# Kernel optimization log

Hardware: AMD Instinct MI355X
Metric: run time of the kernel (lower is better)

The kernel has to match this reference:

```python
import jax, jax.numpy as jnp
import numpy as np
from jax import lax

B, N, H = 256, 512, 256


def setup_inputs() -> dict:
    key = jax.random.key(0)
    ks = jax.random.split(key, 8)
    s = 1.0 / np.sqrt(H)  # torch default init scale ~ U(-1/sqrt(H), 1/sqrt(H))
    return {
        "encoder_outputs": jax.random.normal(ks[0], (B, N, H), dtype=jnp.float32),
        "W_ih": jax.random.uniform(ks[1], (4 * H, H), jnp.float32, -s, s),
        "W_hh": jax.random.uniform(ks[2], (4 * H, H), jnp.float32, -s, s),
        "b_ih": jax.random.uniform(ks[3], (4 * H,), jnp.float32, -s, s),
        "b_hh": jax.random.uniform(ks[4], (4 * H,), jnp.float32, -s, s),
        "W_ref": jax.random.uniform(ks[5], (H, H), jnp.float32, -s, s),
        "W_q": jax.random.uniform(ks[6], (H, H), jnp.float32, -s, s),
        "v": jax.random.uniform(ks[7], (H,), jnp.float32, -s, s),
    }


def reference(encoder_outputs, W_ih, W_hh, b_ih, b_hh, W_ref, W_q, v):
    # Inference path (target_permutation=None): LSTM input at each step is the
    # previous hidden state; mask stays all-ones so masked_fill is a no-op.
    b, n, h = encoder_outputs.shape
    enc_proj = jnp.einsum('bnh,kh->bnk', encoder_outputs, W_ref)  # W_ref(encoder_outputs)

    def step(carry, _):
        hid, cell = carry
        # torch LSTMCell: gates = x W_ih^T + b_ih + h W_hh^T + b_hh, order (i,f,g,o)
        gates = hid @ W_ih.T + b_ih + hid @ W_hh.T + b_hh  # x == hid here
        i, f, g, o = jnp.split(gates, 4, axis=-1)
        cell = jax.nn.sigmoid(f) * cell + jax.nn.sigmoid(i) * jnp.tanh(g)
        hid = jax.nn.sigmoid(o) * jnp.tanh(cell)
        q = hid @ W_q.T                                    # [B,H]
        logits = jnp.tanh(enc_proj + q[:, None, :]) @ v    # [B,N]
        return (hid, cell), logits

    init = (jnp.zeros((b, h), encoder_outputs.dtype),
            jnp.zeros((b, h), encoder_outputs.dtype))
    _, logits_tn = lax.scan(step, init, None, length=n)    # [N,B,N]
    return jnp.transpose(logits_tn, (1, 0, 2))             # [B,N,N]
```

## Files before the change

### kernel.cpp

```cpp
#include <hip/hip_runtime.h>
#include <math.h>


#define CL2 2.8853900817779268f
#define LOG2E 1.4426950408889634f

#define YN0 0.98078528f
#define YN1 0.83146961f
#define YN2 0.55557023f
#define YN3 0.19509032f

#if __has_builtin(__builtin_amdgcn_exp2f)
__device__ __forceinline__ float fast_exp2(float x) { return __builtin_amdgcn_exp2f(x); }
#else
__device__ __forceinline__ float fast_exp2(float x) { return exp2f(x); }
#endif

#if __has_builtin(__builtin_amdgcn_rcpf)
__device__ __forceinline__ float fast_rcp(float x) { return __builtin_amdgcn_rcpf(x); }
#else
__device__ __forceinline__ float fast_rcp(float x) { return 1.0f / x; }
#endif

#if __has_builtin(__builtin_amdgcn_sdot4)
__device__ __forceinline__ int sdot4(int a, int b, int c) {
  return __builtin_amdgcn_sdot4(a, b, c, false);
}
#else
__device__ __forceinline__ int sdot4(int a, int b, int c) {
  c += (int)(signed char)(a)       * (int)(signed char)(b);
  c += (int)(signed char)(a >> 8)  * (int)(signed char)(b >> 8);
  c += (int)(signed char)(a >> 16) * (int)(signed char)(b >> 16);
  c += (int)(signed char)(a >> 24) * (int)(signed char)(b >> 24);
  return c;
}
#endif

typedef _Float16 f16x8 __attribute__((ext_vector_type(8)));
typedef float f32x4 __attribute__((ext_vector_type(4)));

__device__ __forceinline__ f16x8 as_f16x8(float4 x) {
  union { float4 f; f16x8 h; } u; u.f = x; return u.h;
}


__global__ void prep_kernel(const float* __restrict__ Wih, const float* __restrict__ Whh,
                            const float* __restrict__ bih, const float* __restrict__ bhh,
                            const float* __restrict__ Wref,
                            int* __restrict__ wpack, float* __restrict__ bsum,
                            unsigned short* __restrict__ Wrefsw) {
  const int bid = blockIdx.x, tid = threadIdx.x;
  if (bid < 256) {
    const int idx   = bid * 256 + tid;
    const int gidx  = idx & 3;
    const int chunk = (idx >> 2) & 15;
    const int qd    = (idx >> 6) & 255;
    const int sl    = idx >> 14;
    const int gate  = 4 * qd + gidx;
    const int k0    = 64 * sl + 4 * chunk;
    unsigned pk = 0u;
#pragma unroll
    for (int j = 0; j < 4; ++j) {
      float val = Wih[gate * 256 + k0 + j] + Whh[gate * 256 + k0 + j];
      int qi = (int)rintf(val * (127.0f / 0.125f));
      qi = qi > 127 ? 127 : (qi < -127 ? -127 : qi);
      pk |= ((unsigned)(qi & 255)) << (8 * j);
    }
    wpack[idx] = (int)pk;
  } else if (bid < 260) {
    const int g = (bid - 256) * 256 + tid;
    bsum[g] = bih[g] + bhh[g];
  } else {
    const int kcol = bid - 260;
    const int h    = tid;
    union { _Float16 f; unsigned short u; } cv;
    cv.f = (_Float16)Wref[kcol * 256 + h];
    const int unit = ((kcol >> 4) * 8 + (h >> 5)) * 64 + (kcol & 15) + 16 * ((h >> 3) & 3);
    Wrefsw[unit * 8 + (h & 7)] = cv.u;
  }
}

__global__ __launch_bounds__(1024)
__attribute__((amdgpu_waves_per_eu(4, 4)))
void lstm_kernel(
    const int* __restrict__ wpack, const float* __restrict__ bsum,
    float* __restrict__ hid_all) {
  __shared__ int   hb[64];
  __shared__ int   pg[4 * 1028];
  __shared__ float acts[1024];
  const int tid = threadIdx.x;
  const int qd  = tid & 255;
  const int sl  = tid >> 8;

  int w[64];
#pragma unroll
  for (int i = 0; i < 64; ++i) w[i] = wpack[tid * 64 + i];
  const float bias = bsum[tid];
  const int gtype = tid >> 8;
  float cell = 0.0f;

  if (tid < 64) hb[tid] = 0;
  __syncthreads();

  const float SCs = 0.125f / (127.0f * 127.0f);
  const int pgw = sl * 1028 + 4 * qd;
  const int4* hb4 = (const int4*)(hb + sl * 16);

  for (int t = 0; t < 512; ++t) {
    const int4 h0 = hb4[0];
    const int4 h1 = hb4[1];
    const int4 h2 = hb4[2];
    const int4 h3 = hb4[3];
    int a0 = 0, a1 = 0, a2 = 0, a3 = 0;
#define CH(c, hdw)                        \
    a0 = sdot4(w[4*(c)+0], (hdw), a0);    \
    a1 = sdot4(w[4*(c)+1], (hdw), a1);    \
    a2 = sdot4(w[4*(c)+2], (hdw), a2);    \
    a3 = sdot4(w[4*(c)+3], (hdw), a3);
    CH(0,  h0.x) CH(1,  h0.y) CH(2,  h0.z) CH(3,  h0.w)
    CH(4,  h1.x) CH(5,  h1.y) CH(6,  h1.z) CH(7,  h1.w)
    CH(8,  h2.x) CH(9,  h2.y) CH(10, h2.z) CH(11, h2.w)
    CH(12, h3.x) CH(13, h3.y) CH(14, h3.z) CH(15, h3.w)
#undef CH
    *(int4*)&pg[pgw] = make_int4(a0, a1, a2, a3);
    __syncthreads();

    {
      const int s = pg[tid] + pg[1028 + tid] + pg[2056 + tid] + pg[3084 + tid];
      const float gf = fmaf((float)s, SCs, bias);
      float act;
      if (gtype == 2) {
        act = 1.0f - 2.0f * fast_rcp(fast_exp2(CL2 * gf) + 1.0f);
      } else {
        act = fast_rcp(1.0f + fast_exp2(-LOG2E * gf));
      }
      acts[tid] = act;
    }
    __syncthreads();

    if (tid < 256) {
      const float si = acts[tid];
      const float sf = acts[256 + tid];
      const float tg = acts[512 + tid];
      const float so = acts[768 + tid];
      cell = fmaf(sf, cell, si * tg);
      const float tc = 1.0f - 2.0f * fast_rcp(fast_exp2(CL2 * cell) + 1.0f);
      const float hv = so * tc;
      hid_all[t * 256 + tid] = hv;
      int b1 = (int)rintf(hv * 127.0f);
      b1 = b1 > 127 ? 127 : (b1 < -127 ? -127 : b1);
      ((signed char*)hb)[tid] = (signed char)b1;
    }
    __syncthreads();
  }
}

__global__ __launch_bounds__(256) void gproj_kernel(
    const float* __restrict__ hid_all, const float* __restrict__ Wq,
    float* __restrict__ Gsw) {
  __shared__ float hrow[256];
  const int t = blockIdx.x, k = threadIdx.x;
  hrow[k] = hid_all[t * 256 + k];
  __syncthreads();
  const float* wr = Wq + k * 256;
  float acc = 0.0f;
#pragma unroll 8
  for (int h = 0; h < 256; h += 4) {
    const float4 w4 = *(const float4*)(wr + h);
    acc = fmaf(w4.x, hrow[h + 0], acc);
    acc = fmaf(w4.y, hrow[h + 1], acc);
    acc = fmaf(w4.z, hrow[h + 2], acc);
    acc = fmaf(w4.w, hrow[h + 3], acc);
  }
  const float y = fminf(fmaxf(acc, -1.25f), 1.25f);

  const float d0 = y - YN0, d1 = y - YN1, d2 = y - YN2, d3 = y - YN3;
  const float d4 = y + YN3, d5 = y + YN2, d6 = y + YN1, d7 = y + YN0;
  const float w0 = 1.0f/((YN0-YN1)*(YN0-YN2)*(YN0-YN3)*(YN0+YN3)*(YN0+YN2)*(YN0+YN1)*(YN0+YN0));
  const float w1 = 1.0f/((YN1-YN0)*(YN1-YN2)*(YN1-YN3)*(YN1+YN3)*(YN1+YN2)*(YN1+YN1)*(YN1+YN0));
  const float w2 = 1.0f/((YN2-YN0)*(YN2-YN1)*(YN2-YN3)*(YN2+YN3)*(YN2+YN2)*(YN2+YN1)*(YN2+YN0));
  const float w3 = 1.0f/((YN3-YN0)*(YN3-YN1)*(YN3-YN2)*(YN3+YN3)*(YN3+YN2)*(YN3+YN1)*(YN3+YN0));
  const float w4_ = 1.0f/((-YN3-YN0)*(-YN3-YN1)*(-YN3-YN2)*(-YN3-YN3)*(-YN3+YN2)*(-YN3+YN1)*(-YN3+YN0));
  const float w5 = 1.0f/((-YN2-YN0)*(-YN2-YN1)*(-YN2-YN2)*(-YN2-YN3)*(-YN2+YN3)*(-YN2+YN1)*(-YN2+YN0));
  const float w6 = 1.0f/((-YN1-YN0)*(-YN1-YN1)*(-YN1-YN2)*(-YN1-YN3)*(-YN1+YN3)*(-YN1+YN2)*(-YN1+YN0));
  const float w7 = 1.0f/((-YN0-YN0)*(-YN0-YN1)*(-YN0-YN2)*(-YN0-YN3)*(-YN0+YN3)*(-YN0+YN2)*(-YN0+YN1));

  const float P1 = d0, P2 = P1*d1, P3 = P2*d2, P4 = P3*d3, P5 = P4*d4, P6 = P5*d5, P7 = P6*d6;
  const float S6 = d7, S5 = S6*d6, S4 = S5*d5, S3 = S4*d4, S2 = S3*d3, S1 = S2*d2, S0 = S1*d1;

  union { _Float16 h[8]; float4 f; } pk;
  pk.h[0] = (_Float16)(w0 * S0);
  pk.h[1] = (_Float16)(w1 * P1 * S1);
  pk.h[2] = (_Float16)(w2 * P2 * S2);
  pk.h[3] = (_Float16)(w3 * P3 * S3);
  pk.h[4] = (_Float16)(w4_ * P4 * S4);
  pk.h[5] = (_Float16)(w5 * P5 * S5);
  pk.h[6] = (_Float16)(w6 * P6 * S6);
  pk.h[7] = (_Float16)(w7 * P7);

  float4* G4 = (float4*)Gsw;
  G4[((t >> 4) * 64 + (k >> 2)) * 64 + (t & 15) + 16 * (k & 3)] = pk.f;
}

__global__ __launch_bounds__(512)
__attribute__((amdgpu_waves_per_eu(4, 4)))
void main_kernel(
    const float* __restrict__ enc, const float* __restrict__ Wrefsw_,
    const float* __restrict__ v, const float* __restrict__ Gsw,
    float* __restrict__ out) {
  __shared__ _Float16 ep16[64 * 258];
  __shared__ __align__(16) _Float16 ah[2][4][2048];
  __shared__ float vlds[256];
  const int tid = threadIdx.x;
  const int b   = blockIdx.y;
  const int n0  = blockIdx.x * 64;
  const int wv   = tid >> 6;
  const int lane = tid & 63;

  if (tid < 256) vlds[tid] = v[tid];

  {
    const int mt  = wv >> 1;
    const int nh  = wv & 1;
    const int row = lane & 15;
    const int hs8 = (lane >> 4) * 8;
    const float* encb = enc + ((size_t)(b * 512) + n0 + mt * 16 + row) * 256;
    const float4* W4 = (const float4*)Wrefsw_;

    f32x4 C8[8];
#pragma unroll
    for (int i = 0; i < 8; ++i) C8[i] = (f32x4){0.0f, 0.0f, 0.0f, 0.0f};

#pragma unroll
    for (int s = 0; s < 8; ++s) {
      const float4 x0 = *(const float4*)(encb + s * 32 + hs8);
      const float4 x1 = *(const float4*)(encb + s * 32 + hs8 + 4);
      union { _Float16 h[8]; f16x8 vv; } af;
      af.h[0] = (_Float16)x0.x; af.h[1] = (_Float16)x0.y;
      af.h[2] = (_Float16)x0.z; af.h[3] = (_Float16)x0.w;
      af.h[4] = (_Float16)x1.x; af.h[5] = (_Float16)x1.y;
      af.h[6] = (_Float16)x1.z; af.h[7] = (_Float16)x1.w;
#pragma unroll
      for (int nt = 0; nt < 8; ++nt) {
        const int kt = nh * 8 + nt;
        const float4 bf = W4[(kt * 8 + s) * 64 + lane];
        C8[nt] = __builtin_amdgcn_mfma_f32_16x16x32_f16(af.vv, as_f16x8(bf), C8[nt], 0, 0, 0);
      }
    }
#pragma unroll
    for (int nt = 0; nt < 8; ++nt) {
      const int kcol = (nh * 8 + nt) * 16 + (lane & 15);
#pragma unroll
      for (int r = 0; r < 4; ++r) {
        const int n = mt * 16 + (lane >> 4) * 4 + r;
        ep16[n * 258 + kcol] =
            (_Float16)fminf(fmaxf(CL2 * C8[nt][r], -40.0f), 40.0f);
      }
    }
  }

  const int ni  = tid >> 3;
  const int kcl = (tid >> 1) & 3;
  const int rh  = tid & 1;
  const float eA = fast_exp2(CL2 * (rh ? -YN3 : YN0));
  const float eB = fast_exp2(CL2 * (rh ? -YN2 : YN1));
  const float eC = fast_exp2(CL2 * (rh ? -YN1 : YN2));
  const float eD = fast_exp2(CL2 * (rh ? -YN0 : YN3));
  const int lane16 = (ni & 15) + 16 * kcl;
  const int wofs   = ((ni >> 4) * 64 + (lane16 ^ ((lane16 >> 3) & 7))) * 8 + rh * 4;

  auto do_stage = [&](int stage, int j4) {
#pragma unroll
    for (int m = 0; m < 4; ++m) {
      const int kc = j4 * 16 + m * 4 + kcl;
      const float x2 = (float)ep16[ni * 258 + kc];
      const float u  = fast_exp2(x2);
      const float vs = 16.0f * vlds[kc];
      const float m2 = -2.0f * vs;
      union { _Float16 h[4]; uint2 u2; } pk;
      pk.h[0] = (_Float16)fmaf(m2, fast_rcp(fmaf(u, eA, 1.0f)), vs);
      pk.h[1] = (_Float16)fmaf(m2, fast_rcp(fmaf(u, eB, 1.0f)), vs);
      pk.h[2] = (_Float16)fmaf(m2, fast_rcp(fmaf(u, eC, 1.0f)), vs);
      pk.h[3] = (_Float16)fmaf(m2, fast_rcp(fmaf(u, eD, 1.0f)), vs);
      *(uint2*)&ah[stage][m][wofs] = pk.u2;
    }
  };

  __syncthreads();
  do_stage(0, 0);
  __syncthreads();

  const int swl = (lane ^ ((lane >> 3) & 7)) * 8;
  const float4* G4 = (const float4*)Gsw;

  f32x4 C[4][4];
#pragma unroll
  for (int p = 0; p < 4; ++p)
#pragma unroll
    for (int nb = 0; nb < 4; ++nb)
      C[p][nb] = (f32x4){0.0f, 0.0f, 0.0f, 0.0f};

  for (int j = 0; j < 16; ++j) {
    if (j < 15) do_stage((j + 1) & 1, j + 1);

#pragma unroll
    for (int m = 0; m < 4; ++m) {
      const int kb = j * 4 + m;
      const float4 a0 = G4[((wv * 4 + 0) * 64 + kb) * 64 + lane];
      const float4 a1 = G4[((wv * 4 + 1) * 64 + kb) * 64 + lane];
      const float4 a2 = G4[((wv * 4 + 2) * 64 + kb) * 64 + lane];
      const float4 a3 = G4[((wv * 4 + 3) * 64 + kb) * 64 + lane];

      const _Float16* ahr = &ah[j & 1][m][0];
      const f16x8 B0 = *(const f16x8*)(ahr + 0 * 512 + swl);
      const f16x8 B1 = *(const f16x8*)(ahr + 1 * 512 + swl);
      const f16x8 B2 = *(const f16x8*)(ahr + 2 * 512 + swl);
      const f16x8 B3 = *(const f16x8*)(ahr + 3 * 512 + swl);

      C[0][0] = __builtin_amdgcn_mfma_f32_16x16x32_f16(as_f16x8(a0), B0, C[0][0], 0, 0, 0);
      C[0][1] = __builtin_amdgcn_mfma_f32_16x16x32_f16(as_f16x8(a0), B1, C[0][1], 0, 0, 0);
      C[0][2] = __builtin_amdgcn_mfma_f32_16x16x32_f16(as_f16x8(a0), B2, C[0][2], 0, 0, 0);
      C[0][3] = __builtin_amdgcn_mfma_f32_16x16x32_f16(as_f16x8(a0), B3, C[0][3], 0, 0, 0);
      C[1][0] = __builtin_amdgcn_mfma_f32_16x16x32_f16(as_f16x8(a1), B0, C[1][0], 0, 0, 0);
      C[1][1] = __builtin_amdgcn_mfma_f32_16x16x32_f16(as_f16x8(a1), B1, C[1][1], 0, 0, 0);
      C[1][2] = __builtin_amdgcn_mfma_f32_16x16x32_f16(as_f16x8(a1), B2, C[1][2], 0, 0, 0);
      C[1][3] = __builtin_amdgcn_mfma_f32_16x16x32_f16(as_f16x8(a1), B3, C[1][3], 0, 0, 0);
      C[2][0] = __builtin_amdgcn_mfma_f32_16x16x32_f16(as_f16x8(a2), B0, C[2][0], 0, 0, 0);
      C[2][1] = __builtin_amdgcn_mfma_f32_16x16x32_f16(as_f16x8(a2), B1, C[2][1], 0, 0, 0);
      C[2][2] = __builtin_amdgcn_mfma_f32_16x16x32_f16(as_f16x8(a2), B2, C[2][2], 0, 0, 0);
      C[2][3] = __builtin_amdgcn_mfma_f32_16x16x32_f16(as_f16x8(a2), B3, C[2][3], 0, 0, 0);
      C[3][0] = __builtin_amdgcn_mfma_f32_16x16x32_f16(as_f16x8(a3), B0, C[3][0], 0, 0, 0);
      C[3][1] = __builtin_amdgcn_mfma_f32_16x16x32_f16(as_f16x8(a3), B1, C[3][1], 0, 0, 0);
      C[3][2] = __builtin_amdgcn_mfma_f32_16x16x32_f16(as_f16x8(a3), B2, C[3][2], 0, 0, 0);
      C[3][3] = __builtin_amdgcn_mfma_f32_16x16x32_f16(as_f16x8(a3), B3, C[3][3], 0, 0, 0);
    }
    __syncthreads();
  }

  const int trow = (lane >> 4) * 4;
  const int ncol = lane & 15;
#pragma unroll
  for (int p = 0; p < 4; ++p) {
#pragma unroll
    for (int nb = 0; nb < 4; ++nb) {
      size_t base = ((size_t)b * 512 + (size_t)((wv * 4 + p) * 16 + trow)) * 512
                    + n0 + nb * 16 + ncol;
      out[base]        = 0.0625f * C[p][nb][0];
      out[base + 512]  = 0.0625f * C[p][nb][1];
      out[base + 1024] = 0.0625f * C[p][nb][2];
      out[base + 1536] = 0.0625f * C[p][nb][3];
    }
  }
}

extern "C" void kernel_launch(void* const* d_in, const int* in_sizes, int n_in,
                              void* d_out, int out_size, void* d_ws, size_t ws_size,
                              hipStream_t stream) {
  const float* enc  = (const float*)d_in[0];
  const float* Wih  = (const float*)d_in[1];
  const float* Whh  = (const float*)d_in[2];
  const float* bih  = (const float*)d_in[3];
  const float* bhh  = (const float*)d_in[4];
  const float* Wref = (const float*)d_in[5];
  const float* Wq   = (const float*)d_in[6];
  const float* v    = (const float*)d_in[7];
  float* out = (float*)d_out;

  char* ws = (char*)d_ws;
  int*   wpack = (int*)(ws + 0);
  float* bsum  = (float*)(ws + 262144);
  float* hid   = (float*)(ws + 266240);
  float* Gsw   = (float*)(ws + 790528);
  unsigned short* Wrefsw = (unsigned short*)(ws + 2887680);

  prep_kernel<<<516, 256, 0, stream>>>(Wih, Whh, bih, bhh, Wref, wpack, bsum, Wrefsw);
  lstm_kernel<<<1, 1024, 0, stream>>>(wpack, bsum, hid);
  gproj_kernel<<<512, 256, 0, stream>>>(hid, Wq, Gsw);
  dim3 grid(8, 256);
  main_kernel<<<grid, 512, 0, stream>>>(enc, (const float*)Wrefsw, v, Gsw, out);
}
```

Before: 794.9 us.

## Reduce LSTM K-slice partials with wave shuffles instead of shared memory

The weight packing is reordered so the four K-slices of each group of four gate rows sit in adjacent lanes. Partial dot-product sums are then combined with xor shuffles inside the wavefront rather than written to a shared-memory buffer and summed after a barrier. This drops one __syncthreads and the shared-memory round trip from each of the 512 serial recurrence steps. The trade-off is eight extra shuffles per step and a lane-dependent select, and weights are now loaded as int4 vectors.

```diff
diff --git a/kernel.cpp b/kernel.cpp
--- a/kernel.cpp
+++ b/kernel.cpp
@@ -53,11 +53,10 @@
   if (bid < 256) {
     const int idx   = bid * 256 + tid;
     const int gidx  = idx & 3;
-    const int chunk = (idx >> 2) & 15;
-    const int qd    = (idx >> 6) & 255;
-    const int sl    = idx >> 14;
-    const int gate  = 4 * qd + gidx;
-    const int k0    = 64 * sl + 4 * chunk;
+    const int c     = (idx >> 2) & 15;
+    const int tid_l = idx >> 6;
+    const int gate  = (tid_l & ~3) + gidx;
+    const int k0    = 64 * (tid_l & 3) + 4 * c;
     unsigned pk = 0u;
 #pragma unroll
     for (int j = 0; j < 4; ++j) {
@@ -86,24 +85,24 @@
     const int* __restrict__ wpack, const float* __restrict__ bsum,
     float* __restrict__ hid_all) {
   __shared__ int   hb[64];
-  __shared__ int   pg[4 * 1028];
   __shared__ float acts[1024];
   const int tid = threadIdx.x;
-  const int qd  = tid & 255;
-  const int sl  = tid >> 8;
-
-  int w[64];
-#pragma unroll
-  for (int i = 0; i < 64; ++i) w[i] = wpack[tid * 64 + i];
-  const float bias = bsum[tid];
-  const int gtype = tid >> 8;
+  const int sl  = tid & 3;
+
+  const int4* wp = (const int4*)(wpack) + tid * 16;
+  const int4 w0 = wp[0],  w1 = wp[1],  w2 = wp[2],  w3 = wp[3];
+  const int4 w4 = wp[4],  w5 = wp[5],  w6 = wp[6],  w7 = wp[7];
+  const int4 w8 = wp[8],  w9 = wp[9],  wA = wp[10], wB = wp[11];
+  const int4 wC = wp[12], wD = wp[13], wE = wp[14], wF = wp[15];
+
+  const float bias  = bsum[tid];
+  const int   gtype = tid >> 8;
   float cell = 0.0f;
 
   if (tid < 64) hb[tid] = 0;
   __syncthreads();
 
   const float SCs = 0.125f / (127.0f * 127.0f);
-  const int pgw = sl * 1028 + 4 * qd;
   const int4* hb4 = (const int4*)(hb + sl * 16);
 
   for (int t = 0; t < 512; ++t) {
@@ -112,30 +111,27 @@
     const int4 h2 = hb4[2];
     const int4 h3 = hb4[3];
     int a0 = 0, a1 = 0, a2 = 0, a3 = 0;
-#define CH(c, hdw)                        \
-    a0 = sdot4(w[4*(c)+0], (hdw), a0);    \
-    a1 = sdot4(w[4*(c)+1], (hdw), a1);    \
-    a2 = sdot4(w[4*(c)+2], (hdw), a2);    \
-    a3 = sdot4(w[4*(c)+3], (hdw), a3);
-    CH(0,  h0.x) CH(1,  h0.y) CH(2,  h0.z) CH(3,  h0.w)
-    CH(4,  h1.x) CH(5,  h1.y) CH(6,  h1.z) CH(7,  h1.w)
-    CH(8,  h2.x) CH(9,  h2.y) CH(10, h2.z) CH(11, h2.w)
-    CH(12, h3.x) CH(13, h3.y) CH(14, h3.z) CH(15, h3.w)
+#define CH(W, hdw)                    \
+    a0 = sdot4((W).x, (hdw), a0);     \
+    a1 = sdot4((W).y, (hdw), a1);     \
+    a2 = sdot4((W).z, (hdw), a2);     \
+    a3 = sdot4((W).w, (hdw), a3);
+    CH(w0, h0.x) CH(w1, h0.y) CH(w2, h0.z) CH(w3, h0.w)
+    CH(w4, h1.x) CH(w5, h1.y) CH(w6, h1.z) CH(w7, h1.w)
+    CH(w8, h2.x) CH(w9, h2.y) CH(wA, h2.z) CH(wB, h2.w)
+    CH(wC, h3.x) CH(wD, h3.y) CH(wE, h3.z) CH(wF, h3.w)
 #undef CH
-    *(int4*)&pg[pgw] = make_int4(a0, a1, a2, a3);
-    __syncthreads();
-
-    {
-      const int s = pg[tid] + pg[1028 + tid] + pg[2056 + tid] + pg[3084 + tid];
-      const float gf = fmaf((float)s, SCs, bias);
-      float act;
-      if (gtype == 2) {
-        act = 1.0f - 2.0f * fast_rcp(fast_exp2(CL2 * gf) + 1.0f);
-      } else {
-        act = fast_rcp(1.0f + fast_exp2(-LOG2E * gf));
-      }
-      acts[tid] = act;
-    }
+    a0 += __shfl_xor(a0, 1); a0 += __shfl_xor(a0, 2);
+    a1 += __shfl_xor(a1, 1); a1 += __shfl_xor(a1, 2);
+    a2 += __shfl_xor(a2, 1); a2 += __shfl_xor(a2, 2);
+    a3 += __shfl_xor(a3, 1); a3 += __shfl_xor(a3, 2);
+    const int s = (sl == 0) ? a0 : (sl == 1) ? a1 : (sl == 2) ? a2 : a3;
+
+    const float gf = fmaf((float)s, SCs, bias);
+    float act;
+    if (gtype == 2) act = 1.0f - 2.0f * fast_rcp(fast_exp2(CL2 * gf) + 1.0f);
+    else            act = fast_rcp(1.0f + fast_exp2(-LOG2E * gf));
+    acts[tid] = act;
     __syncthreads();
 
     if (tid < 256) {
```

Result: slower. 841.1 us (+5.8%).
